# Performance work log

Hardware: AMD Instinct MI355X
Metric: run time of the kernel (lower is better)

The kernel has to match this reference:

```python
import jax, jax.numpy as jnp
import numpy as np

AGENT, WIN = 6, 7

def _rel_pos_index(d, h, w):
    # same construction as the torch buffer `relative_position_index`
    coords = np.stack(np.meshgrid(np.arange(d), np.arange(h), np.arange(w), indexing='ij'))
    cf = coords.reshape(3, -1)                                   # [3, S]
    rc = (cf[:, :, None] - cf[:, None, :]).transpose(1, 2, 0).astype(np.int64)
    rc[:, :, 0] += d - 1; rc[:, :, 1] += h - 1; rc[:, :, 2] += w - 1
    rc[:, :, 0] *= (2 * h - 1) * (2 * w - 1)
    rc[:, :, 1] *= (2 * w - 1)
    return jnp.asarray(rc.sum(-1))                               # [S, S]

def setup_inputs() -> dict:
    key = jax.random.key(0)
    ks = jax.random.split(key, 11)
    b, L, X, Y, w1, w2, dim = 2, AGENT, 8, 8, WIN, WIN, 256
    heads, ch, nt = 8, 32, 2
    table = (2 * L - 1) * (2 * w1 - 1) * (2 * w2 - 1)
    f = lambda k, s: (0.02 * jax.random.normal(k, s)).astype(jnp.float32)
    return dict(
        x=jax.random.normal(ks[0], (b, L, X, Y, w1, w2, dim), jnp.float32),
        Wq=f(ks[1], (nt, dim, dim)), bq=f(ks[2], (nt, dim)),
        Wk=f(ks[3], (nt, dim, dim)), bk=f(ks[4], (nt, dim)),
        Wv=f(ks[5], (nt, dim, dim)), bv=f(ks[6], (nt, dim)),
        rel_att=f(ks[7], (nt * nt, heads, ch, ch)),
        rel_msg=f(ks[8], (nt * nt, heads, ch, ch)),
        bias_table=f(ks[9], (table, heads)),
        Wo=f(ks[10], (dim, dim)),
        agent_type=1,
    )

def reference(x, Wq, bq, Wk, bk, Wv, bv, rel_att, rel_msg, bias_table, Wo, agent_type):
    b, L, X, Y, w1, w2, dim = x.shape
    heads, ch = rel_att.shape[1], rel_att.shape[2]
    nt = Wq.shape[0]
    scale = ch ** -0.5
    # types = [0] + (agent_size-1)*[type], identical across batch (as in forward)
    types = jnp.concatenate([jnp.zeros(1, jnp.int32),
                             jnp.full((L - 1,), agent_type, jnp.int32)])

    def proj(W, bias):
        # type-indexed per-agent linear (gathered batched matmul instead of python loops)
        y = jnp.einsum('blxyuvd,lde->blxyuve', x, W[types])
        y = y + bias[types][None, :, None, None, None, None, :]
        # -> [b, n=(X*Y) windows, m heads, L agents, p=(w1*w2) tokens, c]
        return y.reshape(b, L, X * Y, w1 * w2, heads, ch).transpose(0, 2, 4, 1, 3, 5)

    q = proj(Wq, bq) * scale
    k = proj(Wk, bk)
    v = proj(Wv, bv)

    # relation weights gathered by (src_type, dst_type) pair: [m, L, L, c, c]
    rel = types[:, None] * nt + types[None, :]
    w_att = rel_att[rel].transpose(2, 0, 1, 3, 4)
    w_msg = rel_msg[rel].transpose(2, 0, 1, 3, 4)

    # bilinear hetero attention scores, grouped by agent pair (i,j)
    sim = jnp.einsum('bnmipc,mijcf,bnmjqf->bnmipjq', q, w_att, k)
    S, n = L * w1 * w2, X * Y
    sim = sim.reshape(b, n, heads, S, S)
    idx = _rel_pos_index(L, w1, w2)                                # [S, S] static
    sim = sim + bias_table[idx].transpose(2, 0, 1)                 # + [m, S, S] rel-pos bias
    attn = jax.nn.softmax(sim, axis=-1).reshape(b, n, heads, L, w1 * w2, L, w1 * w2)

    # relation-transformed messages, then attention-weighted aggregation
    vt = jnp.einsum('mijcf,bnmjqf->bnmijqc', w_msg, v)
    out = jnp.einsum('bnmipjq,bnmijqc->bnmipc', attn, vt)
    # [b, n, m, L, p, c] -> [b, L, X, Y, w1, w2, dim]
    out = out.transpose(0, 3, 1, 4, 2, 5).reshape(b, L, X, Y, w1, w2, dim)
    return out @ Wo.T
```

## Files before the change

### kernel.cpp

```cpp
#include <hip/hip_runtime.h>
#include <hip/hip_bf16.h>

typedef __hip_bfloat16 bf16;
typedef unsigned short u16;
typedef short bf16x8 __attribute__((ext_vector_type(8)));
typedef float f32x4  __attribute__((ext_vector_type(4)));

#define BB    2
#define LL    6
#define NWIN  64
#define PP    49
#define DIMM  256
#define HEADS 8
#define CHN   32
#define SS    294
#define ASTRIDE 264
#define BSTRIDE 304
#define VSTRIDE 308
#define PSTRIDE 164

__device__ __forceinline__ u16 bfbits(float x) { return __bfloat16_as_ushort(__float2bfloat16(x)); }
__device__ __forceinline__ f32x4 mfma16(bf16x8 a, bf16x8 b, f32x4 c) {
    return __builtin_amdgcn_mfma_f32_16x16x32_bf16(a, b, c, 0, 0, 0);
}

__global__ __launch_bounds__(256) void k_prep(
    const float* __restrict__ Wq, const float* __restrict__ Wk, const float* __restrict__ Wv,
    const float* __restrict__ Wo, const float* __restrict__ ra, const float* __restrict__ rm,
    const float* __restrict__ bt,
    u16* __restrict__ wT, u16* __restrict__ Wob, u16* __restrict__ raT, u16* __restrict__ rmb,
    float* __restrict__ biasM)
{
    const int blk = blockIdx.x;
    if (blk < 1792) {
        const int idx = blk*256 + threadIdx.x;
        if (idx >= 7*65536) return;
        const int mat = idx >> 16, rem = idx & 65535;
        if (mat < 6) {
            const int tz = mat >> 1, t = mat & 1;
            const int e = rem >> 8, d = rem & 255;
            const float* W = (tz == 0 ? Wq : tz == 1 ? Wk : Wv);
            wT[mat*65536 + rem] = bfbits(W[t*65536 + d*256 + e]);
        } else {
            Wob[rem] = bfbits(Wo[rem]);
        }
    } else if (blk < 1920) {
        const int idx = (blk - 1792)*256 + threadIdx.x;
        if (idx < 4*HEADS*CHN*CHN) {
            const int pm = idx >> 10, cf = idx & 1023, c = cf >> 5, f = cf & 31;
            raT[(pm << 10) + (f << 5) + c] = bfbits(ra[idx]);
            rmb[idx] = bfbits(rm[idx]);
        }
    } else {
        const int idx = (blk - 1920)*256 + threadIdx.x;
        if (idx < HEADS*SS*BSTRIDE) {
            const int m = idx / (SS*BSTRIDE);
            const int rem = idx % (SS*BSTRIDE);
            const int s1 = rem / BSTRIDE, s2 = rem % BSTRIDE;
            float val = 0.f;
            if (s2 < SS) {
                const int i1 = s1/49, p1 = s1 - i1*49, h1 = p1/7, w1 = p1 - h1*7;
                const int j2 = s2/49, p2 = s2 - j2*49, h2 = p2/7, w2 = p2 - h2*7;
                const int rc = i1*169 + h1*13 + w1, cc = j2*169 + h2*13 + w2;
                val = bt[(rc - cc + 929)*8 + m];
            }
            biasM[idx] = val;
        }
    }
}

__global__ __launch_bounds__(256) void k_qkv2(
    const float* __restrict__ x, const u16* __restrict__ wT,
    const float* __restrict__ bq, const float* __restrict__ bk, const float* __restrict__ bv,
    const int* __restrict__ atype,
    u16* __restrict__ q, u16* __restrict__ k, u16* __restrict__ v)
{
    __shared__ __align__(16) u16 As[64*ASTRIDE];
    const int tid = threadIdx.x;
    const int w = tid >> 6, lane = tid & 63;
    const int g4 = lane >> 4, c16 = lane & 15;
    const int bid = blockIdx.x;
    const int nwin = bid & 63;
    const int l = (bid >> 6) % LL;
    const int b = bid / (LL*NWIN);

    const float4* xp = (const float4*)(x + (size_t)bid * (PP*DIMM));
    for (int idx = tid; idx < 49*64; idx += 256) {
        const int row = idx >> 6, c4 = idx & 63;
        const float4 xv = xp[idx];
        ushort4 h;
        h.x = bfbits(xv.x); h.y = bfbits(xv.y); h.z = bfbits(xv.z); h.w = bfbits(xv.w);
        *(ushort4*)&As[row*ASTRIDE + c4*4] = h;
    }
    const ushort4 z4 = {0, 0, 0, 0};
    for (int idx = tid; idx < 15*66; idx += 256) {
        const int row = 49 + idx/66, c4 = idx%66;
        *(ushort4*)&As[row*ASTRIDE + c4*4] = z4;
    }
    __syncthreads();

    const int t = (l == 0) ? 0 : atype[0];
    const f32x4 zero4 = {0.f, 0.f, 0.f, 0.f};

    for (int tz = 0; tz < 3; ++tz) {
        const u16* WT = wT + (size_t)(tz*2 + t)*65536;
        const float* bias = (tz == 0 ? bq : tz == 1 ? bk : bv) + t*DIMM;
        u16* dst = (tz == 0 ? q : tz == 1 ? k : v);
        const float scale = (tz == 0) ? 0.17677669529663687f : 1.0f;

        f32x4 acc[4][4];
        #pragma unroll
        for (int mm = 0; mm < 4; ++mm)
            #pragma unroll
            for (int nn = 0; nn < 4; ++nn) acc[mm][nn] = zero4;

        for (int ks = 0; ks < 8; ++ks) {
            bf16x8 a[4], bb[4];
            #pragma unroll
            for (int mm = 0; mm < 4; ++mm)
                a[mm] = *(const bf16x8*)&As[(mm*16 + c16)*ASTRIDE + ks*32 + g4*8];
            #pragma unroll
            for (int nn = 0; nn < 4; ++nn)
                bb[nn] = *(const bf16x8*)&WT[(size_t)(w*64 + nn*16 + c16)*256 + ks*32 + g4*8];
            #pragma unroll
            for (int mm = 0; mm < 4; ++mm)
                #pragma unroll
                for (int nn = 0; nn < 4; ++nn)
                    acc[mm][nn] = mfma16(a[mm], bb[nn], acc[mm][nn]);
        }

        #pragma unroll
        for (int nn = 0; nn < 4; ++nn) {
            const int col = w*64 + nn*16 + c16;
            const float bval = bias[col];
            const int head = col >> 5, c = col & 31;
            const size_t base = (((size_t)(b*NWIN + nwin)*HEADS + head)*SS + l*PP)*CHN + c;
            #pragma unroll
            for (int mm = 0; mm < 4; ++mm) {
                #pragma unroll
                for (int r = 0; r < 4; ++r) {
                    const int row = mm*16 + g4*4 + r;
                    if (row < PP)
                        dst[base + (size_t)row*CHN] = bfbits((acc[mm][nn][r] + bval)*scale);
                }
            }
        }
    }
}

__global__ __launch_bounds__(256) void k_attn(
    const u16* __restrict__ q, const u16* __restrict__ kk_, const u16* __restrict__ v,
    const u16* __restrict__ raT, const u16* __restrict__ rmb,
    const float* __restrict__ biasM, const int* __restrict__ atype,
    u16* __restrict__ o_pre)
{
    __shared__ __align__(16) u16 vT[32*VSTRIDE + 32];
    __shared__ __align__(16) u16 vT0[32*72];
    __shared__ __align__(16) u16 wbuf[4*16*PSTRIDE];

    const int tid  = threadIdx.x;
    const int w    = tid >> 6;
    const int lane = tid & 63;
    const int g4   = lane >> 4;
    const int c16  = lane & 15;
    const int bid  = blockIdx.x;
    const int m    = bid & 7;
    const int nwin = (bid >> 3) & 63;
    const int b    = bid >> 9;
    const int at   = atype[0];

    const size_t slab = (size_t)bid * (SS*CHN);
    const u16* qs  = q   + slab;
    const u16* ksg = kk_ + slab;
    const u16* vsg = v   + slab;
    const float* bm = biasM + (size_t)m*(SS*BSTRIDE);

    u16* wb = wbuf + w*(16*PSTRIDE);

    for (int idx = tid; idx < 32*(VSTRIDE - SS) + 32; idx += 256) {
        if (idx < 32*(VSTRIDE - SS)) {
            const int f = idx / (VSTRIDE - SS), c = idx % (VSTRIDE - SS);
            vT[f*VSTRIDE + SS + c] = 0;
        } else {
            vT[32*VSTRIDE + (idx - 32*(VSTRIDE - SS))] = 0;
        }
    }
    for (int idx = tid; idx < 32*15; idx += 256) vT0[(idx/15)*72 + 49 + (idx%15)] = 0;
    for (int idx = tid; idx < SS*CHN/2; idx += 256) {
        const int s2 = idx >> 4;
        const int f2 = (idx & 15) << 1;
        const unsigned int val = *(const unsigned int*)(vsg + s2*CHN + f2);
        const u16 v0 = (u16)(val & 0xffff), v1 = (u16)(val >> 16);
        vT[f2*VSTRIDE + s2]     = v0;
        vT[(f2+1)*VSTRIDE + s2] = v1;
        if (s2 < 49) { vT0[f2*72 + s2] = v0; vT0[(f2+1)*72 + s2] = v1; }
    }
    __syncthreads();

    const f32x4 zero4 = {0.f, 0.f, 0.f, 0.f};

    for (int job = w; job < 20; job += 4) {
        const int tile = (job == 19) ? 3 : job;
        const int tiv  = (job <= 3) ? 0 : at;
        const int pair0 = tiv*2;
        const int pair1 = tiv*2 + at;

        const int rowA = tile*16 + c16;
        const bf16x8 aq = *(const bf16x8*)(qs + rowA*CHN + g4*8);
        {
            const u16* base0 = raT + (pair0*HEADS + m)*1024;
            const u16* base1 = raT + (pair1*HEADS + m)*1024;
            const bf16x8 b00 = *(const bf16x8*)(base0 + (c16     )*32 + g4*8);
            const bf16x8 b01 = *(const bf16x8*)(base0 + (16 + c16)*32 + g4*8);
            const bf16x8 b10 = *(const bf16x8*)(base1 + (c16     )*32 + g4*8);
            const bf16x8 b11 = *(const bf16x8*)(base1 + (16 + c16)*32 + g4*8);
            const f32x4 cqw00 = mfma16(aq, b00, zero4);
            const f32x4 cqw01 = mfma16(aq, b01, zero4);
            const f32x4 cqw10 = mfma16(aq, b10, zero4);
            const f32x4 cqw11 = mfma16(aq, b11, zero4);
            #pragma unroll
            for (int r = 0; r < 4; ++r) {
                const int row = g4*4 + r;
                wb[row*72 +      c16] = bfbits(cqw00[r]);
                wb[row*72 + 16 + c16] = bfbits(cqw01[r]);
                wb[row*72 + 32 + c16] = bfbits(cqw10[r]);
                wb[row*72 + 48 + c16] = bfbits(cqw11[r]);
            }
        }
        const bf16x8 A0 = *(const bf16x8*)(wb + c16*72 +      g4*8);
        const bf16x8 A1 = *(const bf16x8*)(wb + c16*72 + 32 + g4*8);

        f32x4 acc[19];
        #pragma unroll
        for (int t = 0; t < 3; ++t) {
            const bf16x8 bk = *(const bf16x8*)(ksg + (t*16 + c16)*CHN + g4*8);
            acc[t] = mfma16(A0, bk, zero4);
        }
        {
            const bf16x8 bk = *(const bf16x8*)(ksg + (3*16 + c16)*CHN + g4*8);
            const f32x4 cA = mfma16(A0, bk, zero4);
            const f32x4 cB = mfma16(A1, bk, zero4);
            #pragma unroll
            for (int r = 0; r < 4; ++r) acc[3][r] = (c16 == 0) ? cA[r] : cB[r];
        }
        #pragma unroll
        for (int t = 4; t < 19; ++t) {
            const bf16x8 bk = *(const bf16x8*)(ksg + (t*16 + c16)*CHN + g4*8);
            acc[t] = mfma16(A1, bk, zero4);
        }

        int boff[4];
        #pragma unroll
        for (int r = 0; r < 4; ++r) {
            const int s1r = tile*16 + g4*4 + r;
            const int s1c = (s1r < SS) ? s1r : 293;
            boff[r] = s1c*BSTRIDE;
        }
        #pragma unroll
        for (int t = 0; t < 19; ++t)
            #pragma unroll
            for (int r = 0; r < 4; ++r)
                acc[t][r] += bm[boff[r] + t*16 + c16];
        #pragma unroll
        for (int r = 0; r < 4; ++r)
            acc[18][r] = (c16 < 6) ? acc[18][r] : -1e30f;

        float mx[4], sm[4];
        #pragma unroll
        for (int r = 0; r < 4; ++r) mx[r] = -1e30f;
        #pragma unroll
        for (int t = 0; t < 19; ++t)
            #pragma unroll
            for (int r = 0; r < 4; ++r) mx[r] = fmaxf(mx[r], acc[t][r]);
        #pragma unroll
        for (int off = 1; off < 16; off <<= 1)
            #pragma unroll
            for (int r = 0; r < 4; ++r) mx[r] = fmaxf(mx[r], __shfl_xor(mx[r], off));
        #pragma unroll
        for (int r = 0; r < 4; ++r) sm[r] = 0.f;
        #pragma unroll
        for (int t = 0; t < 19; ++t)
            #pragma unroll
            for (int r = 0; r < 4; ++r) { const float e = __expf(acc[t][r] - mx[r]); acc[t][r] = e; sm[r] += e; }
        #pragma unroll
        for (int off = 1; off < 16; off <<= 1)
            #pragma unroll
            for (int r = 0; r < 4; ++r) sm[r] += __shfl_xor(sm[r], off);
        #pragma unroll
        for (int r = 0; r < 4; ++r) {
            const float inv = 1.0f / sm[r];
            #pragma unroll
            for (int t = 0; t < 19; ++t) acc[t][r] *= inv;
        }

        f32x4 aggF0a = zero4, aggF0b = zero4, aggF1a = zero4, aggF1b = zero4;
        f32x4 agg00 = zero4, agg01 = zero4;
        bf16x8 asave0, asave1;
        #pragma unroll
        for (int t = 0; t < 10; ++t)
            #pragma unroll
            for (int r = 0; r < 4; ++r)
                wb[(g4*4 + r)*PSTRIDE + t*16 + c16] = bfbits(acc[t][r]);
        #pragma unroll
        for (int ks = 0; ks < 5; ++ks) {
            const bf16x8 ap  = *(const bf16x8*)(wb + c16*PSTRIDE + ks*32 + g4*8);
            const bf16x8 bv0 = *(const bf16x8*)(vT + (c16     )*VSTRIDE + ks*32 + g4*8);
            const bf16x8 bv1 = *(const bf16x8*)(vT + (16 + c16)*VSTRIDE + ks*32 + g4*8);
            if (ks & 1) { aggF0b = mfma16(ap, bv0, aggF0b); aggF1b = mfma16(ap, bv1, aggF1b); }
            else        { aggF0a = mfma16(ap, bv0, aggF0a); aggF1a = mfma16(ap, bv1, aggF1a); }
            if (ks == 0) asave0 = ap;
            if (ks == 1) asave1 = ap;
        }

        #pragma unroll
        for (int t2 = 0; t2 < 9; ++t2)
            #pragma unroll
            for (int r = 0; r < 4; ++r)
                wb[(g4*4 + r)*PSTRIDE + t2*16 + c16] = bfbits(acc[10 + t2][r]);
        #pragma unroll
        for (int r = 0; r < 4; ++r)
            wb[(g4*4 + r)*PSTRIDE + 9*16 + c16] = 0;
        #pragma unroll
        for (int ks2 = 0; ks2 < 5; ++ks2) {
            const int ks = 5 + ks2;
            const bf16x8 ap  = *(const bf16x8*)(wb + c16*PSTRIDE + ks2*32 + g4*8);
            const bf16x8 bv0 = *(const bf16x8*)(vT + (c16     )*VSTRIDE + ks*32 + g4*8);
            const bf16x8 bv1 = *(const bf16x8*)(vT + (16 + c16)*VSTRIDE + ks*32 + g4*8);
            if (ks2 & 1) { aggF0b = mfma16(ap, bv0, aggF0b); aggF1b = mfma16(ap, bv1, aggF1b); }
            else         { aggF0a = mfma16(ap, bv0, aggF0a); aggF1a = mfma16(ap, bv1, aggF1a); }
        }

        {
            const bf16x8 b00 = *(const bf16x8*)(vT0 + (c16     )*72 +      g4*8);
            const bf16x8 b01 = *(const bf16x8*)(vT0 + (16 + c16)*72 +      g4*8);
            const bf16x8 b10 = *(const bf16x8*)(vT0 + (c16     )*72 + 32 + g4*8);
            const bf16x8 b11 = *(const bf16x8*)(vT0 + (16 + c16)*72 + 32 + g4*8);
            agg00 = mfma16(asave0, b00, agg00); agg00 = mfma16(asave1, b10, agg00);
            agg01 = mfma16(asave0, b01, agg01); agg01 = mfma16(asave1, b11, agg01);
        }
        const f32x4 aggF0 = aggF0a + aggF0b;
        const f32x4 aggF1 = aggF1a + aggF1b;
        const f32x4 agg10 = aggF0 - agg00;
        const f32x4 agg11 = aggF1 - agg01;

        #pragma unroll
        for (int r = 0; r < 4; ++r) {
            const int row = g4*4 + r;
            wb[row*72 +      c16] = bfbits(agg00[r]);
            wb[row*72 + 16 + c16] = bfbits(agg01[r]);
            wb[row*72 + 32 + c16] = bfbits(agg10[r]);
            wb[row*72 + 48 + c16] = bfbits(agg11[r]);
        }
        const bf16x8 aA0 = *(const bf16x8*)(wb + c16*72 +      g4*8);
        const bf16x8 aA1 = *(const bf16x8*)(wb + c16*72 + 32 + g4*8);
        const u16* mb0 = rmb + (pair0*HEADS + m)*1024;
        const u16* mb1 = rmb + (pair1*HEADS + m)*1024;
        const bf16x8 bm00 = *(const bf16x8*)(mb0 + (c16     )*32 + g4*8);
        const bf16x8 bm01 = *(const bf16x8*)(mb0 + (16 + c16)*32 + g4*8);
        const bf16x8 bm10 = *(const bf16x8*)(mb1 + (c16     )*32 + g4*8);
        const bf16x8 bm11 = *(const bf16x8*)(mb1 + (16 + c16)*32 + g4*8);
        f32x4 out0 = mfma16(aA0, bm00, zero4); out0 = mfma16(aA1, bm10, out0);
        f32x4 out1 = mfma16(aA0, bm01, zero4); out1 = mfma16(aA1, bm11, out1);

        #pragma unroll
        for (int r = 0; r < 4; ++r) {
            const int s1row = tile*16 + g4*4 + r;
            bool valid = (s1row < SS);
            if (job == 3)  valid = valid && (s1row == 48);
            if (job == 19) valid = valid && (s1row >= 49);
            if (valid) {
                const int i = s1row / 49, p = s1row - i*49;
                const size_t rb = ((size_t)((b*LL + i)*NWIN + nwin)*PP + p)*DIMM + m*CHN;
                o_pre[rb + c16]      = bfbits(out0[r]);
                o_pre[rb + 16 + c16] = bfbits(out1[r]);
            }
        }
    }
}

__global__ __launch_bounds__(256) void k_out2(
    const u16* __restrict__ pre, const u16* __restrict__ Wob,
    float* __restrict__ out)
{
    __shared__ __align__(16) u16 As[64*ASTRIDE];
    const int tid = threadIdx.x;
    const int w = tid >> 6, lane = tid & 63;
    const int g4 = lane >> 4, c16 = lane & 15;
    const int bid = blockIdx.x;

    const uint4* pp = (const uint4*)(pre + (size_t)bid * (PP*DIMM));
    for (int idx = tid; idx < 49*32; idx += 256) {
        const int row = idx >> 5, c8 = idx & 31;
        *(uint4*)&As[row*ASTRIDE + c8*8] = pp[idx];
    }
    const ushort4 z4 = {0, 0, 0, 0};
    for (int idx = tid; idx < 15*66; idx += 256) {
        const int row = 49 + idx/66, c4 = idx%66;
        *(ushort4*)&As[row*ASTRIDE + c4*4] = z4;
    }
    __syncthreads();

    const f32x4 zero4 = {0.f, 0.f, 0.f, 0.f};
    f32x4 acc[4][4];
    #pragma unroll
    for (int mm = 0; mm < 4; ++mm)
        #pragma unroll
        for (int nn = 0; nn < 4; ++nn) acc[mm][nn] = zero4;

    for (int ks = 0; ks < 8; ++ks) {
        bf16x8 a[4], bb[4];
        #pragma unroll
        for (int mm = 0; mm < 4; ++mm)
            a[mm] = *(const bf16x8*)&As[(mm*16 + c16)*ASTRIDE + ks*32 + g4*8];
        #pragma unroll
        for (int nn = 0; nn < 4; ++nn)
            bb[nn] = *(const bf16x8*)&Wob[(size_t)(w*64 + nn*16 + c16)*256 + ks*32 + g4*8];
        #pragma unroll
        for (int mm = 0; mm < 4; ++mm)
            #pragma unroll
            for (int nn = 0; nn < 4; ++nn)
                acc[mm][nn] = mfma16(a[mm], bb[nn], acc[mm][nn]);
    }

    float* op = out + (size_t)bid * (PP*DIMM);
    #pragma unroll
    for (int nn = 0; nn < 4; ++nn) {
        const int col = w*64 + nn*16 + c16;
        #pragma unroll
        for (int mm = 0; mm < 4; ++mm) {
            #pragma unroll
            for (int r = 0; r < 4; ++r) {
                const int row = mm*16 + g4*4 + r;
                if (row < PP) op[(size_t)row*DIMM + col] = acc[mm][nn][r];
            }
        }
    }
}

extern "C" void kernel_launch(void* const* d_in, const int* in_sizes, int n_in,
                              void* d_out, int out_size, void* d_ws, size_t ws_size,
                              hipStream_t stream)
{
    (void)in_sizes; (void)n_in; (void)out_size; (void)ws_size;
    const float* x        = (const float*)d_in[0];
    const float* Wq       = (const float*)d_in[1];
    const float* bq       = (const float*)d_in[2];
    const float* Wk       = (const float*)d_in[3];
    const float* bk       = (const float*)d_in[4];
    const float* Wv       = (const float*)d_in[5];
    const float* bv       = (const float*)d_in[6];
    const float* rel_att  = (const float*)d_in[7];
    const float* rel_msg  = (const float*)d_in[8];
    const float* bias_tab = (const float*)d_in[9];
    const float* Wo       = (const float*)d_in[10];
    const int*   atype    = (const int*)d_in[11];
    float* out = (float*)d_out;

    char* ws = (char*)d_ws;
    u16* wT     = (u16*)ws;
    u16* Wob    = (u16*)(ws + 786432);
    u16* raT    = (u16*)(ws + 917504);
    u16* rmb    = (u16*)(ws + 983040);
    float* biasM= (float*)(ws + 1048576);
    u16* qb     = (u16*)(ws + 3908608);
    u16* kb     = (u16*)(ws + 3908608 + 1ull*19267584);
    u16* vb     = (u16*)(ws + 3908608 + 2ull*19267584);
    u16* o_preb = (u16*)(ws + 3908608 + 3ull*19267584);

    k_prep<<<4713, 256, 0, stream>>>(Wq, Wk, Wv, Wo, rel_att, rel_msg, bias_tab,
                                     wT, Wob, raT, rmb, biasM);
    k_qkv2<<<BB*LL*NWIN, 256, 0, stream>>>(x, wT, bq, bk, bv, atype, qb, kb, vb);
    k_attn<<<BB*NWIN*HEADS, 256, 0, stream>>>(qb, kb, vb, raT, rmb, biasM, atype, o_preb);
    k_out2<<<BB*LL*NWIN, 256, 0, stream>>>(o_preb, Wob, out);
}
```

Measured before the change: 235.2 us.

## Stream scores through two passes instead of holding all score tiles in registers

The score MFMAs are recomputed in two passes: a first pass finds only the row max, and a second pass exponentiates, accumulates the sum and writes unnormalized probabilities straight to LDS. Normalization is deferred to after the PV aggregation. This removes the 19-tile accumulator array, cutting register pressure so occupancy can rise. The separate vT0 shared buffer is dropped by masking the A operand and reading the first 49 columns from vT directly, and the LDS strides change. The cost is the score MFMAs and K loads being done twice, plus a change in rounding because bf16 probabilities are now unnormalized.

Result: slower. 390.4 us (+66.0%).

```diff
diff --git a/kernel.cpp b/kernel.cpp
--- a/kernel.cpp
+++ b/kernel.cpp
@@ -16,8 +16,8 @@
 #define SS    294
 #define ASTRIDE 264
 #define BSTRIDE 304
-#define VSTRIDE 308
-#define PSTRIDE 164
+#define VSTRIDE 296
+#define PSTRIDE 168
 
 __device__ __forceinline__ u16 bfbits(float x) { return __bfloat16_as_ushort(__float2bfloat16(x)); }
 __device__ __forceinline__ f32x4 mfma16(bf16x8 a, bf16x8 b, f32x4 c) {
@@ -154,8 +154,7 @@
     const float* __restrict__ biasM, const int* __restrict__ atype,
     u16* __restrict__ o_pre)
 {
-    __shared__ __align__(16) u16 vT[32*VSTRIDE + 32];
-    __shared__ __align__(16) u16 vT0[32*72];
+    __shared__ __align__(16) u16 vT[32*VSTRIDE + 48];
     __shared__ __align__(16) u16 wbuf[4*16*PSTRIDE];
 
     const int tid  = threadIdx.x;
@@ -177,27 +176,21 @@
 
     u16* wb = wbuf + w*(16*PSTRIDE);
 
-    for (int idx = tid; idx < 32*(VSTRIDE - SS) + 32; idx += 256) {
-        if (idx < 32*(VSTRIDE - SS)) {
-            const int f = idx / (VSTRIDE - SS), c = idx % (VSTRIDE - SS);
-            vT[f*VSTRIDE + SS + c] = 0;
-        } else {
-            vT[32*VSTRIDE + (idx - 32*(VSTRIDE - SS))] = 0;
-        }
-    }
-    for (int idx = tid; idx < 32*15; idx += 256) vT0[(idx/15)*72 + 49 + (idx%15)] = 0;
+    for (int idx = tid; idx < 112; idx += 256) {
+        if (idx < 64) vT[(idx >> 1)*VSTRIDE + 294 + (idx & 1)] = 0;
+        else          vT[32*VSTRIDE + (idx - 64)] = 0;
+    }
     for (int idx = tid; idx < SS*CHN/2; idx += 256) {
         const int s2 = idx >> 4;
         const int f2 = (idx & 15) << 1;
         const unsigned int val = *(const unsigned int*)(vsg + s2*CHN + f2);
-        const u16 v0 = (u16)(val & 0xffff), v1 = (u16)(val >> 16);
-        vT[f2*VSTRIDE + s2]     = v0;
-        vT[(f2+1)*VSTRIDE + s2] = v1;
-        if (s2 < 49) { vT0[f2*72 + s2] = v0; vT0[(f2+1)*72 + s2] = v1; }
+        vT[f2*VSTRIDE + s2]     = (u16)(val & 0xffff);
+        vT[(f2+1)*VSTRIDE + s2] = (u16)(val >> 16);
     }
     __syncthreads();
 
     const f32x4 zero4 = {0.f, 0.f, 0.f, 0.f};
+    const bf16x8 zero8 = {0, 0, 0, 0, 0, 0, 0, 0};
 
     for (int job = w; job < 20; job += 4) {
         const int tile = (job == 19) ? 3 : job;
@@ -230,25 +223,6 @@
         const bf16x8 A0 = *(const bf16x8*)(wb + c16*72 +      g4*8);
         const bf16x8 A1 = *(const bf16x8*)(wb + c16*72 + 32 + g4*8);
 
-        f32x4 acc[19];
-        #pragma unroll
-        for (int t = 0; t < 3; ++t) {
-            const bf16x8 bk = *(const bf16x8*)(ksg + (t*16 + c16)*CHN + g4*8);
-            acc[t] = mfma16(A0, bk, zero4);
-        }
-        {
-            const bf16x8 bk = *(const bf16x8*)(ksg + (3*16 + c16)*CHN + g4*8);
-            const f32x4 cA = mfma16(A0, bk, zero4);
-            const f32x4 cB = mfma16(A1, bk, zero4);
-            #pragma unroll
-            for (int r = 0; r < 4; ++r) acc[3][r] = (c16 == 0) ? cA[r] : cB[r];
-        }
-        #pragma unroll
-        for (int t = 4; t < 19; ++t) {
-            const bf16x8 bk = *(const bf16x8*)(ksg + (t*16 + c16)*CHN + g4*8);
-            acc[t] = mfma16(A1, bk, zero4);
-        }
-
         int boff[4];
         #pragma unroll
         for (int r = 0; r < 4; ++r) {
@@ -256,51 +230,61 @@
             const int s1c = (s1r < SS) ? s1r : 293;
             boff[r] = s1c*BSTRIDE;
         }
-        #pragma unroll
-        for (int t = 0; t < 19; ++t)
-            #pragma unroll
-            for (int r = 0; r < 4; ++r)
-                acc[t][r] += bm[boff[r] + t*16 + c16];
-        #pragma unroll
-        for (int r = 0; r < 4; ++r)
-            acc[18][r] = (c16 < 6) ? acc[18][r] : -1e30f;
-
-        float mx[4], sm[4];
+
+        float mx[4];
         #pragma unroll
         for (int r = 0; r < 4; ++r) mx[r] = -1e30f;
         #pragma unroll
-        for (int t = 0; t < 19; ++t)
-            #pragma unroll
-            for (int r = 0; r < 4; ++r) mx[r] = fmaxf(mx[r], acc[t][r]);
+        for (int t = 0; t < 19; ++t) {
+            const bf16x8 bk = *(const bf16x8*)(ksg + (t*16 + c16)*CHN + g4*8);
+            f32x4 s;
+            if (t < 3)       s = mfma16(A0, bk, zero4);
+            else if (t == 3) {
+                const f32x4 cA = mfma16(A0, bk, zero4);
+                const f32x4 cB = mfma16(A1, bk, zero4);
+                #pragma unroll
+                for (int r = 0; r < 4; ++r) s[r] = (c16 == 0) ? cA[r] : cB[r];
+            }
+            else             s = mfma16(A1, bk, zero4);
+            #pragma unroll
+            for (int r = 0; r < 4; ++r) {
+                float v = s[r] + bm[boff[r] + t*16 + c16];
+                if (t == 18) v = (c16 < 6) ? v : -1e30f;
+                mx[r] = fmaxf(mx[r], v);
+            }
+        }
         #pragma unroll
         for (int off = 1; off < 16; off <<= 1)
             #pragma unroll
             for (int r = 0; r < 4; ++r) mx[r] = fmaxf(mx[r], __shfl_xor(mx[r], off));
+
+        float sm[4];
         #pragma unroll
         for (int r = 0; r < 4; ++r) sm[r] = 0.f;
-        #pragma unroll
-        for (int t = 0; t < 19; ++t)
-            #pragma unroll
-            for (int r = 0; r < 4; ++r) { const float e = __expf(acc[t][r] - mx[r]); acc[t][r] = e; sm[r] += e; }
-        #pragma unroll
-        for (int off = 1; off < 16; off <<= 1)
-            #pragma unroll
-            for (int r = 0; r < 4; ++r) sm[r] += __shfl_xor(sm[r], off);
-        #pragma unroll
-        for (int r = 0; r < 4; ++r) {
-            const float inv = 1.0f / sm[r];
-            #pragma unroll
-            for (int t = 0; t < 19; ++t) acc[t][r] *= inv;
+
+        #pragma unroll
+        for (int t = 0; t < 10; ++t) {
+            const bf16x8 bk = *(const bf16x8*)(ksg + (t*16 + c16)*CHN + g4*8);
+            f32x4 s;
+            if (t < 3)       s = mfma16(A0, bk, zero4);
+            else if (t == 3) {
+                const f32x4 cA = mfma16(A0, bk, zero4);
+                const f32x4 cB = mfma16(A1, bk, zero4);
+                #pragma unroll
+                for (int r = 0; r < 4; ++r) s[r] = (c16 == 0) ? cA[r] : cB[r];
+            }
+            else             s = mfma16(A1, bk, zero4);
+            #pragma unroll
+            for (int r = 0; r < 4; ++r) {
+                const float e = __expf(s[r] + bm[boff[r] + t*16 + c16] - mx[r]);
+                sm[r] += e;
+                wb[(g4*4 + r)*PSTRIDE + t*16 + c16] = bfbits(e);
+            }
         }
 
         f32x4 aggF0a = zero4, aggF0b = zero4, aggF1a = zero4, aggF1b = zero4;
         f32x4 agg00 = zero4, agg01 = zero4;
         bf16x8 asave0, asave1;
-        #pragma unroll
-        for (int t = 0; t < 10; ++t)
-            #pragma unroll
-            for (int r = 0; r < 4; ++r)
-                wb[(g4*4 + r)*PSTRIDE + t*16 + c16] = bfbits(acc[t][r]);
         #pragma unroll
         for (int ks = 0; ks < 5; ++ks) {
             const bf16x8 ap  = *(const bf16x8*)(wb + c16*PSTRIDE + ks*32 + g4*8);
@@ -311,15 +295,36 @@
             if (ks == 0) asave0 = ap;
             if (ks == 1) asave1 = ap;
         }
-
-        #pragma unroll
-        for (int t2 = 0; t2 < 9; ++t2)
-            #pragma unroll
-            for (int r = 0; r < 4; ++r)
-                wb[(g4*4 + r)*PSTRIDE + t2*16 + c16] = bfbits(acc[10 + t2][r]);
+        {
+            bf16x8 a1m;
+            if (g4 < 2)       a1m = asave1;
+            else if (g4 == 2) { a1m = zero8; a1m[0] = asave1[0]; }
+            else              a1m = zero8;
+            const bf16x8 b00 = *(const bf16x8*)(vT + (c16     )*VSTRIDE +      g4*8);
+            const bf16x8 b01 = *(const bf16x8*)(vT + (16 + c16)*VSTRIDE +      g4*8);
+            const bf16x8 b10 = *(const bf16x8*)(vT + (c16     )*VSTRIDE + 32 + g4*8);
+            const bf16x8 b11 = *(const bf16x8*)(vT + (16 + c16)*VSTRIDE + 32 + g4*8);
+            agg00 = mfma16(asave0, b00, agg00); agg00 = mfma16(a1m, b10, agg00);
+            agg01 = mfma16(asave0, b01, agg01); agg01 = mfma16(a1m, b11, agg01);
+        }
+
+        #pragma unroll
+        for (int t2 = 0; t2 < 9; ++t2) {
+            const int t = 10 + t2;
+            const bf16x8 bk = *(const bf16x8*)(ksg + (t*16 + c16)*CHN + g4*8);
+            const f32x4 s = mfma16(A1, bk, zero4);
+            #pragma unroll
+            for (int r = 0; r < 4; ++r) {
+                float e = __expf(s[r] + bm[boff[r] + t*16 + c16] - mx[r]);
+                if (t2 == 8) e = (c16 < 6) ? e : 0.f;
+                sm[r] += e;
+                wb[(g4*4 + r)*PSTRIDE + t2*16 + c16] = bfbits(e);
+            }
+        }
         #pragma unroll
         for (int r = 0; r < 4; ++r)
             wb[(g4*4 + r)*PSTRIDE + 9*16 + c16] = 0;
+
         #pragma unroll
         for (int ks2 = 0; ks2 < 5; ++ks2) {
             const int ks = 5 + ks2;
@@ -330,24 +335,28 @@
             else         { aggF0a = mfma16(ap, bv0, aggF0a); aggF1a = mfma16(ap, bv1, aggF1a); }
         }
 
-        {
-            const bf16x8 b00 = *(const bf16x8*)(vT0 + (c16     )*72 +      g4*8);
-            const bf16x8 b01 = *(const bf16x8*)(vT0 + (16 + c16)*72 +      g4*8);
-            const bf16x8 b10 = *(const bf16x8*)(vT0 + (c16     )*72 + 32 + g4*8);
-            const bf16x8 b11 = *(const bf16x8*)(vT0 + (16 + c16)*72 + 32 + g4*8);
-            agg00 = mfma16(asave0, b00, agg00); agg00 = mfma16(asave1, b10, agg00);
-            agg01 = mfma16(asave0, b01, agg01); agg01 = mfma16(asave1, b11, agg01);
-        }
-        const f32x4 aggF0 = aggF0a + aggF0b;
-        const f32x4 aggF1 = aggF1a + aggF1b;
-        const f32x4 agg10 = aggF0 - agg00;
-        const f32x4 agg11 = aggF1 - agg01;
+        #pragma unroll
+        for (int off = 1; off < 16; off <<= 1)
+            #pragma unroll
+            for (int r = 0; r < 4; ++r) sm[r] += __shfl_xor(sm[r], off);
+
+        f32x4 agg0s0, agg0s1, agg10, agg11;
+        #pragma unroll
+        for (int r = 0; r < 4; ++r) {
+            const float inv = 1.0f / sm[r];
+            const float f0 = (aggF0a[r] + aggF0b[r]);
+            const float f1 = (aggF1a[r] + aggF1b[r]);
+            agg0s0[r] = agg00[r]*inv;
+            agg0s1[r] = agg01[r]*inv;
+            agg10[r]  = (f0 - agg00[r])*inv;
+            agg11[r]  = (f1 - agg01[r])*inv;
+        }
 
         #pragma unroll
         for (int r = 0; r < 4; ++r) {
             const int row = g4*4 + r;
-            wb[row*72 +      c16] = bfbits(agg00[r]);
-            wb[row*72 + 16 + c16] = bfbits(agg01[r]);
+            wb[row*72 +      c16] = bfbits(agg0s0[r]);
+            wb[row*72 + 16 + c16] = bfbits(agg0s1[r]);
             wb[row*72 + 32 + c16] = bfbits(agg10[r]);
             wb[row*72 + 48 + c16] = bfbits(agg11[r]);
         }
```
